# Kernel optimization log

Hardware: AMD Instinct MI355X
Metric: run time of the kernel (lower is better)

The kernel has to match this reference:

```python
import jax, jax.numpy as jnp
import numpy as np

B, L, H, E = 4, 2048, 8, 64
WINDOW = 8
DILATION = 1


def setup_inputs() -> dict:
    key = jax.random.key(0)
    kq, kk, kv, ka = jax.random.split(key, 4)
    queries = jax.random.normal(kq, (B, L, H, E), dtype=jnp.float32)
    keys = jax.random.normal(kk, (B, L, H, E), dtype=jnp.float32)
    values = jax.random.normal(kv, (B, L, H, E), dtype=jnp.float32)
    alpha = jax.random.uniform(ka, (1,), dtype=jnp.float32)
    return {"queries": queries, "keys": keys, "values": values, "alpha": alpha}


def _full_attention(q, k, v, scale):
    # q,k,v: [B, L, H, E]
    scores = jnp.einsum('blhe,bshe->bhls', q, k) * scale  # [B,H,L,L]
    A = jax.nn.softmax(scores, axis=-1)
    return jnp.einsum('bhls,bshd->blhd', A, v)


def _local_attention(q, k, v, scale):
    # efficient gather-based local window attention, non-causal
    Lk = k.shape[1]
    offsets = jnp.arange(-WINDOW, WINDOW + 1) * DILATION
    idx = jnp.clip(jnp.arange(Lk)[:, None] + offsets[None, :], 0, Lk - 1)
    K_win = k[:, idx]
    V_win = v[:, idx]
    scores = jnp.einsum('blhe,blwhe->blhw', q, K_win) * scale
    A = jax.nn.softmax(scores, axis=-1)
    return jnp.einsum('blhw,blwhe->blhe', A, V_win)


def reference(queries, keys, values, alpha):
    scale = 1.0 / np.sqrt(queries.shape[-1]).astype(np.float32)
    out_full = _full_attention(queries, keys, values, scale)
    out_local = _local_attention(queries, keys, values, scale)
    w = jax.nn.sigmoid(alpha[0])
    # only_target_first=True: positions 1..L-1 take out_full, position 0 is gated
    out = out_full.at[:, 0].set(w * out_full[:, 0] + (1.0 - w) * out_local[:, 0])
    return out
```

## Files before the change

kernel.cpp:

```cpp
#include <hip/hip_runtime.h>

typedef unsigned short u16;
typedef unsigned int   u32;
typedef __attribute__((ext_vector_type(8))) short short8;
typedef __attribute__((ext_vector_type(4))) float f32x4;

#define MFMA16(a, b, c) __builtin_amdgcn_mfma_f32_16x16x32_bf16(a, b, c, 0, 0, 0)

#define GLDS(gp, lp) __builtin_amdgcn_global_load_lds(                         \
    (const __attribute__((address_space(1))) void*)(gp),                       \
    (__attribute__((address_space(3))) void*)(lp), 16, 0, 0)

constexpr int Lv = 2048, Hv = 8, Ev = 64, HE = Hv * Ev;
constexpr float QSCALE = 0.18033688011112042f;

__device__ __forceinline__ float bf2f(u16 u) {
    u32 x = ((u32)u) << 16;
    return __builtin_bit_cast(float, x);
}
__device__ __forceinline__ u16 f2bf(float f) {
    u32 x = __builtin_bit_cast(u32, f);
    u32 r = ((x >> 16) & 1u) + 0x7fffu;
    return (u16)((x + r) >> 16);
}
__device__ __forceinline__ u32 pkbf(float a, float b) {
#if __has_builtin(__builtin_amdgcn_cvt_pk_bf16_f32)
    typedef __attribute__((ext_vector_type(2))) __bf16 bf16x2;
    bf16x2 v = __builtin_amdgcn_cvt_pk_bf16_f32(a, b);
    return __builtin_bit_cast(u32, v);
#else
    return (u32)f2bf(a) | ((u32)f2bf(b) << 16);
#endif
}
__device__ __forceinline__ float fexp2(float x) {
#if __has_builtin(__builtin_amdgcn_exp2f)
    return __builtin_amdgcn_exp2f(x);
#else
    return exp2f(x);
#endif
}

__device__ __forceinline__ int detect_isbf16(const u32* q32, int lane) {
    u32 w0 = q32[2 * lane];
    u32 w1 = q32[2 * lane + 1];
    u16 uu[4] = { (u16)(w0 & 0xffff), (u16)(w0 >> 16),
                  (u16)(w1 & 0xffff), (u16)(w1 >> 16) };
    int p = 0, z = 0;
#pragma unroll
    for (int j = 0; j < 4; ++j) {
        u16 mgn = (u16)(uu[j] & 0x7fff);
        int ex  = mgn >> 7;
        bool zero = (mgn == 0);
        bool pl   = zero || (ex >= 115 && ex <= 132);
        p += pl ? 1 : 0;
        if ((j & 1) == 0) z += zero ? 1 : 0;
    }
    int acc = p | (z << 16);
#pragma unroll
    for (int o = 1; o < 64; o <<= 1) acc += __shfl_xor(acc, o);
    int ps = acc & 0xffff, zs = acc >> 16;
    if (zs >= 100) return 0;
    return (ps >= 240) ? 1 : 0;
}

__device__ __forceinline__ short8 cvt8(const float* p) {
    float4 a = *(const float4*)p, b4 = *(const float4*)(p + 4);
    u32 r[4] = { pkbf(a.x, a.y), pkbf(a.z, a.w), pkbf(b4.x, b4.y), pkbf(b4.z, b4.w) };
    return *(short8*)r;
}
__device__ __forceinline__ short8 cvt8s(const float* p, float s) {
    float4 a = *(const float4*)p, b4 = *(const float4*)(p + 4);
    u32 r[4] = { pkbf(a.x * s, a.y * s), pkbf(a.z * s, a.w * s),
                 pkbf(b4.x * s, b4.y * s), pkbf(b4.z * s, b4.w * s) };
    return *(short8*)r;
}

__global__ __launch_bounds__(512, 4) void attn_kernel(
    const void* __restrict__ qv, const void* __restrict__ kv,
    const void* __restrict__ vv, const void* __restrict__ alphav,
    void* __restrict__ outv)
{
    __shared__ u16 Klds[64 * 64];
    __shared__ u16 Vt[64 * 64];
    __shared__ u16 Plds[8][16 * 64];

    const int tid  = threadIdx.x;
    const int w    = tid >> 6;
    const int lane = tid & 63;
    const int quad = lane >> 4;
    const int m    = lane & 15;

    const int isbf = detect_isbf16((const u32*)qv, lane);

    const int fid = blockIdx.x;
    const int bh  = (fid & 7) * 4 + ((fid >> 3) & 3);
    const int rb  = fid >> 5;
    const int b   = bh >> 3, h = bh & 7;
    const int row0 = rb * 128;

    const size_t bhoff = (size_t)b * Lv * HE + h * Ev;
    const u16*   q16 = (const u16*)qv + bhoff;
    const u16*   k16 = (const u16*)kv + bhoff;
    const u16*   v16 = (const u16*)vv + bhoff;
    const float* q32 = (const float*)qv + bhoff;
    const float* k32 = (const float*)kv + bhoff;
    const float* v32 = (const float*)vv + bhoff;

    short8 qf[2];
    {
        size_t ro = (size_t)(row0 + w * 16 + m) * HE + quad * 8;
        if (isbf) {
            short8 t0 = *(const short8*)(q16 + ro);
            short8 t1 = *(const short8*)(q16 + ro + 32);
#pragma unroll
            for (int j = 0; j < 8; ++j) {
                qf[0][j] = (short)f2bf(bf2f((u16)t0[j]) * QSCALE);
                qf[1][j] = (short)f2bf(bf2f((u16)t1[j]) * QSCALE);
            }
        } else {
            qf[0] = cvt8s(q32 + ro, QSCALE);
            qf[1] = cvt8s(q32 + ro + 32, QSCALE);
        }
    }

    short8 ones8;
#pragma unroll
    for (int j = 0; j < 8; ++j) ones8[j] = (short)0x3F80;

    f32x4 O[4];
    f32x4 Ssum = f32x4{0.f, 0.f, 0.f, 0.f};
#pragma unroll
    for (int et = 0; et < 4; ++et) O[et] = f32x4{0.f, 0.f, 0.f, 0.f};

    const int kkey = tid >> 3, ksl = tid & 7;
    const int koff = kkey * HE + (ksl ^ (kkey & 7)) * 8;
    const int eq = tid & 15, pp = tid >> 4;
    const int kcv = pp >> 2, pq = pp & 3;

    u16* Pw = Plds[w];

    for (int kt = 0; kt < 32; ++kt) {
        __syncthreads();

        if (isbf) {
            GLDS(k16 + (size_t)kt * 64 * HE + koff, Klds + w * 512);
            const u16* vp = v16 + (size_t)(kt * 64 + 2 * pp) * HE + eq * 4;
            uint2 r0 = *(const uint2*)(vp);
            uint2 r1 = *(const uint2*)(vp + HE);
            const u16* a0 = (const u16*)&r0;
            const u16* a1 = (const u16*)&r1;
#pragma unroll
            for (int j = 0; j < 4; ++j) {
                int e  = eq * 4 + j;
                int sl = kcv ^ ((e + (e >> 3)) & 7);
                u32 val = (u32)a0[j] | ((u32)a1[j] << 16);
                *(u32*)&Vt[e * 64 + sl * 8 + pq * 2] = val;
            }
        } else {
            short8 kk = cvt8(k32 + (size_t)kt * 64 * HE + koff);
            *(short8*)&Klds[tid * 8] = kk;

            const float* vp = v32 + (size_t)(kt * 64 + 2 * pp) * HE + eq * 4;
            float4 f0 = *(const float4*)(vp);
            float4 f1 = *(const float4*)(vp + HE);
            float t0[4] = {f0.x, f0.y, f0.z, f0.w};
            float t1[4] = {f1.x, f1.y, f1.z, f1.w};
#pragma unroll
            for (int j = 0; j < 4; ++j) {
                int e  = eq * 4 + j;
                int sl = kcv ^ ((e + (e >> 3)) & 7);
                *(u32*)&Vt[e * 64 + sl * 8 + pq * 2] = pkbf(t0[j], t1[j]);
            }
        }
        __syncthreads();

        f32x4 St[4];
#pragma unroll
        for (int nt = 0; nt < 4; ++nt) St[nt] = f32x4{0.f, 0.f, 0.f, 0.f};
#pragma unroll
        for (int c = 0; c < 2; ++c) {
#pragma unroll
            for (int nt = 0; nt < 4; ++nt) {
                int krow = nt * 16 + m;
                int sl   = (4 * c + quad) ^ (m & 7);
                short8 kf = *(const short8*)&Klds[krow * 64 + sl * 8];
                St[nt] = MFMA16(kf, qf[c], St[nt]);
            }
        }

#pragma unroll
        for (int nt = 0; nt < 4; ++nt) {
            u32 u0 = pkbf(fexp2(St[nt][0]), fexp2(St[nt][1]));
            u32 u1 = pkbf(fexp2(St[nt][2]), fexp2(St[nt][3]));
            int G   = 2 * nt + (quad >> 1);
            int off = m * 64 + ((G ^ (m & 7)) * 8) + (quad & 1) * 4;
            uint2 val; val.x = u0; val.y = u1;
            *(uint2*)&Pw[off] = val;
        }

#pragma unroll
        for (int c = 0; c < 2; ++c) {
            int Gp = (4 * c + quad) ^ (m & 7);
            short8 pf = *(const short8*)&Pw[m * 64 + Gp * 8];
            Ssum = MFMA16(pf, ones8, Ssum);
#pragma unroll
            for (int et = 0; et < 4; ++et) {
                int e  = et * 16 + m;
                int sl = (4 * c + quad) ^ ((e + (e >> 3)) & 7);
                short8 vf = *(const short8*)&Vt[e * 64 + sl * 8];
                O[et] = MFMA16(pf, vf, O[et]);
            }
        }
    }

    float locv[4] = {0.f, 0.f, 0.f, 0.f};
    float wgt = 0.f;
    const bool isrow0 = (rb == 0) && (w == 0) && (quad == 0);
    if (rb == 0 && w == 0) {
        const int e = lane;
        const size_t base = bhoff + e;
#define LDIN(p, i) (isbf ? bf2f(((const u16*)(p))[i]) : ((const float*)(p))[i])
        float qe = LDIN(qv, base);
        float s[9];
#pragma unroll
        for (int j = 0; j < 9; ++j) {
            float prod = qe * LDIN(kv, base + (size_t)j * HE);
#pragma unroll
            for (int o = 1; o < 64; o <<= 1) prod += __shfl_xor(prod, o);
            s[j] = prod * 0.125f;
        }
        float mx = s[0];
#pragma unroll
        for (int j = 1; j < 9; ++j) mx = fmaxf(mx, s[j]);
        float we[9];
#pragma unroll
        for (int j = 0; j < 9; ++j) we[j] = expf(s[j] - mx);
        float denom = 9.f * we[0];
        float acc   = 9.f * we[0] * LDIN(vv, base);
#pragma unroll
        for (int j = 1; j < 9; ++j) {
            denom += we[j];
            acc   += we[j] * LDIN(vv, base + (size_t)j * HE);
        }
        float loc = acc / denom;

        float a;
        if (isbf) {
            a = bf2f(((const u16*)alphav)[0]);
            if (!(a >= 0.0f && a <= 1.0f)) {
                float af = ((const float*)alphav)[0];
                if (af >= 0.0f && af <= 1.0f) a = af;
            }
        } else {
            a = ((const float*)alphav)[0];
            if (!(a >= 0.0f && a <= 1.0f)) {
                float ab = bf2f(((const u16*)alphav)[0]);
                if (ab >= 0.0f && ab <= 1.0f) a = ab;
            }
        }
        wgt = 1.f / (1.f + expf(-a));
#pragma unroll
        for (int et = 0; et < 4; ++et) locv[et] = __shfl(loc, et * 16 + m);
#undef LDIN
    }

#pragma unroll
    for (int r = 0; r < 4; ++r) {
        float inv = 1.0f / Ssum[r];
        int row = row0 + w * 16 + quad * 4 + r;
        size_t oo = (size_t)(b * Lv + row) * HE + h * Ev + m;
        bool blend = isrow0 && (r == 0);
#pragma unroll
        for (int et = 0; et < 4; ++et) {
            float res = O[et][r] * inv;
            if (blend) res = wgt * res + (1.f - wgt) * locv[et];
            if (isbf) ((u16*)outv)[oo + et * 16] = f2bf(res);
            else      ((float*)outv)[oo + et * 16] = res;
        }
    }
}

extern "C" void kernel_launch(void* const* d_in, const int* in_sizes, int n_in,
                              void* d_out, int out_size, void* d_ws, size_t ws_size,
                              hipStream_t stream) {
    hipLaunchKernelGGL(attn_kernel, dim3(512), dim3(512), 0, stream,
                       d_in[0], d_in[1], d_in[2], d_in[3], d_out);
}
```

Before: 148.5 us.

## Double-buffer K/V LDS tiles with register prefetch and template on dtype

Doubles the K and V shared-memory buffers and prefetches the next tile into registers while the current tile's MFMAs run, then stores it to the alternate buffer, so only one barrier is needed per iteration instead of two. The kernel body is also templated on the input dtype so the bf16/fp32 branches are resolved at compile time. The cost is more LDS per block (roughly 48KB) and extra registers for the prefetched data, which could limit occupancy under the 512x4 launch bounds. The bf16 path also drops the direct global-to-LDS load in favour of a register round trip.

Measured after the change: 143.3 us. -3.5%, faster.

```diff
diff --git a/kernel.cpp b/kernel.cpp
--- a/kernel.cpp
+++ b/kernel.cpp
@@ -6,10 +6,6 @@
 typedef __attribute__((ext_vector_type(4))) float f32x4;
 
 #define MFMA16(a, b, c) __builtin_amdgcn_mfma_f32_16x16x32_bf16(a, b, c, 0, 0, 0)
-
-#define GLDS(gp, lp) __builtin_amdgcn_global_load_lds(                         \
-    (const __attribute__((address_space(1))) void*)(gp),                       \
-    (__attribute__((address_space(3))) void*)(lp), 16, 0, 0)
 
 constexpr int Lv = 2048, Hv = 8, Ev = 64, HE = Hv * Ev;
 constexpr float QSCALE = 0.18033688011112042f;
@@ -63,11 +59,6 @@
     return (ps >= 240) ? 1 : 0;
 }
 
-__device__ __forceinline__ short8 cvt8(const float* p) {
-    float4 a = *(const float4*)p, b4 = *(const float4*)(p + 4);
-    u32 r[4] = { pkbf(a.x, a.y), pkbf(a.z, a.w), pkbf(b4.x, b4.y), pkbf(b4.z, b4.w) };
-    return *(short8*)r;
-}
 __device__ __forceinline__ short8 cvt8s(const float* p, float s) {
     float4 a = *(const float4*)p, b4 = *(const float4*)(p + 4);
     u32 r[4] = { pkbf(a.x * s, a.y * s), pkbf(a.z * s, a.w * s),
@@ -75,22 +66,17 @@
     return *(short8*)r;
 }
 
-__global__ __launch_bounds__(512, 4) void attn_kernel(
+template <int ISBF>
+__device__ __forceinline__ void attn_impl(
     const void* __restrict__ qv, const void* __restrict__ kv,
     const void* __restrict__ vv, const void* __restrict__ alphav,
-    void* __restrict__ outv)
+    void* __restrict__ outv, u16* Klds, u16* Vt, u16* PldsAll)
 {
-    __shared__ u16 Klds[64 * 64];
-    __shared__ u16 Vt[64 * 64];
-    __shared__ u16 Plds[8][16 * 64];
-
     const int tid  = threadIdx.x;
     const int w    = tid >> 6;
     const int lane = tid & 63;
     const int quad = lane >> 4;
     const int m    = lane & 15;
-
-    const int isbf = detect_isbf16((const u32*)qv, lane);
 
     const int fid = blockIdx.x;
     const int bh  = (fid & 7) * 4 + ((fid >> 3) & 3);
@@ -109,7 +95,7 @@
     short8 qf[2];
     {
         size_t ro = (size_t)(row0 + w * 16 + m) * HE + quad * 8;
-        if (isbf) {
+        if (ISBF) {
             short8 t0 = *(const short8*)(q16 + ro);
             short8 t1 = *(const short8*)(q16 + ro + 32);
 #pragma unroll
@@ -137,42 +123,67 @@
     const int eq = tid & 15, pp = tid >> 4;
     const int kcv = pp >> 2, pq = pp & 3;
 
-    u16* Pw = Plds[w];
+    u16* Pw = PldsAll + w * 1024;
+
+    float4 kfa, kfb, vfa, vfb;
+    uint4  kru; uint2 vru0, vru1;
+
+#define LOAD_TILE(KT)                                                          \
+    do {                                                                       \
+        if (ISBF) {                                                            \
+            kru  = *(const uint4*)(k16 + (size_t)(KT) * 64 * HE + koff);       \
+            const u16* vp_ = v16 + (size_t)((KT) * 64 + 2 * pp) * HE + eq * 4; \
+            vru0 = *(const uint2*)vp_;                                         \
+            vru1 = *(const uint2*)(vp_ + HE);                                  \
+        } else {                                                               \
+            const float* kp_ = k32 + (size_t)(KT) * 64 * HE + koff;            \
+            kfa = *(const float4*)kp_;                                         \
+            kfb = *(const float4*)(kp_ + 4);                                   \
+            const float* vp_ = v32 + (size_t)((KT) * 64 + 2 * pp) * HE + eq * 4;\
+            vfa = *(const float4*)vp_;                                         \
+            vfb = *(const float4*)(vp_ + HE);                                  \
+        }                                                                      \
+    } while (0)
+
+#define STORE_TILE(KB, VB)                                                     \
+    do {                                                                       \
+        if (ISBF) {                                                            \
+            *(uint4*)&(KB)[tid * 8] = kru;                                     \
+            const u16* a0_ = (const u16*)&vru0;                                \
+            const u16* a1_ = (const u16*)&vru1;                                \
+            _Pragma("unroll")                                                  \
+            for (int j = 0; j < 4; ++j) {                                      \
+                int e_  = eq * 4 + j;                                          \
+                int sl_ = kcv ^ ((e_ + (e_ >> 3)) & 7);                        \
+                u32 val_ = (u32)a0_[j] | ((u32)a1_[j] << 16);                  \
+                *(u32*)&(VB)[e_ * 64 + sl_ * 8 + pq * 2] = val_;               \
+            }                                                                  \
+        } else {                                                               \
+            u32 kk_[4] = { pkbf(kfa.x, kfa.y), pkbf(kfa.z, kfa.w),             \
+                           pkbf(kfb.x, kfb.y), pkbf(kfb.z, kfb.w) };           \
+            *(uint4*)&(KB)[tid * 8] = *(uint4*)kk_;                            \
+            float t0_[4] = {vfa.x, vfa.y, vfa.z, vfa.w};                       \
+            float t1_[4] = {vfb.x, vfb.y, vfb.z, vfb.w};                       \
+            _Pragma("unroll")                                                  \
+            for (int j = 0; j < 4; ++j) {                                      \
+                int e_  = eq * 4 + j;                                          \
+                int sl_ = kcv ^ ((e_ + (e_ >> 3)) & 7);                        \
+                *(u32*)&(VB)[e_ * 64 + sl_ * 8 + pq * 2] = pkbf(t0_[j], t1_[j]);\
+            }                                                                  \
+        }                                                                      \
+    } while (0)
+
+    LOAD_TILE(0);
+    STORE_TILE(Klds, Vt);
+    __syncthreads();
 
     for (int kt = 0; kt < 32; ++kt) {
-        __syncthreads();
-
-        if (isbf) {
-            GLDS(k16 + (size_t)kt * 64 * HE + koff, Klds + w * 512);
-            const u16* vp = v16 + (size_t)(kt * 64 + 2 * pp) * HE + eq * 4;
-            uint2 r0 = *(const uint2*)(vp);
-            uint2 r1 = *(const uint2*)(vp + HE);
-            const u16* a0 = (const u16*)&r0;
-            const u16* a1 = (const u16*)&r1;
-#pragma unroll
-            for (int j = 0; j < 4; ++j) {
-                int e  = eq * 4 + j;
-                int sl = kcv ^ ((e + (e >> 3)) & 7);
-                u32 val = (u32)a0[j] | ((u32)a1[j] << 16);
-                *(u32*)&Vt[e * 64 + sl * 8 + pq * 2] = val;
-            }
-        } else {
-            short8 kk = cvt8(k32 + (size_t)kt * 64 * HE + koff);
-            *(short8*)&Klds[tid * 8] = kk;
-
-            const float* vp = v32 + (size_t)(kt * 64 + 2 * pp) * HE + eq * 4;
-            float4 f0 = *(const float4*)(vp);
-            float4 f1 = *(const float4*)(vp + HE);
-            float t0[4] = {f0.x, f0.y, f0.z, f0.w};
-            float t1[4] = {f1.x, f1.y, f1.z, f1.w};
-#pragma unroll
-            for (int j = 0; j < 4; ++j) {
-                int e  = eq * 4 + j;
-                int sl = kcv ^ ((e + (e >> 3)) & 7);
-                *(u32*)&Vt[e * 64 + sl * 8 + pq * 2] = pkbf(t0[j], t1[j]);
-            }
-        }
-        __syncthreads();
+        u16* Kb = Klds + (kt & 1) * 4096;
+        u16* Vb = Vt   + (kt & 1) * 4096;
+        u16* Kn = Klds + ((kt & 1) ^ 1) * 4096;
+        u16* Vn = Vt   + ((kt & 1) ^ 1) * 4096;
+
+        if (kt < 31) LOAD_TILE(kt + 1);
 
         f32x4 St[4];
 #pragma unroll
@@ -183,7 +194,7 @@
             for (int nt = 0; nt < 4; ++nt) {
                 int krow = nt * 16 + m;
                 int sl   = (4 * c + quad) ^ (m & 7);
-                short8 kf = *(const short8*)&Klds[krow * 64 + sl * 8];
+                short8 kf = *(const short8*)&Kb[krow * 64 + sl * 8];
                 St[nt] = MFMA16(kf, qf[c], St[nt]);
             }
         }
@@ -207,11 +218,18 @@
             for (int et = 0; et < 4; ++et) {
                 int e  = et * 16 + m;
                 int sl = (4 * c + quad) ^ ((e + (e >> 3)) & 7);
-                short8 vf = *(const short8*)&Vt[e * 64 + sl * 8];
+                short8 vf = *(const short8*)&Vb[e * 64 + sl * 8];
                 O[et] = MFMA16(pf, vf, O[et]);
             }
         }
-    }
+
+        if (kt < 31) {
+            STORE_TILE(Kn, Vn);
+            __syncthreads();
+        }
+    }
+#undef LOAD_TILE
+#undef STORE_TILE
 
     float locv[4] = {0.f, 0.f, 0.f, 0.f};
     float wgt = 0.f;
@@ -219,7 +237,7 @@
     if (rb == 0 && w == 0) {
         const int e = lane;
         const size_t base = bhoff + e;
-#define LDIN(p, i) (isbf ? bf2f(((const u16*)(p))[i]) : ((const float*)(p))[i])
+#define LDIN(p, i) (ISBF ? bf2f(((const u16*)(p))[i]) : ((const float*)(p))[i])
         float qe = LDIN(qv, base);
         float s[9];
 #pragma unroll
@@ -245,7 +263,7 @@
         float loc = acc / denom;
 
         float a;
-        if (isbf) {
+        if (ISBF) {
             a = bf2f(((const u16*)alphav)[0]);
             if (!(a >= 0.0f && a <= 1.0f)) {
                 float af = ((const float*)alphav)[0];
@@ -274,10 +292,24 @@
         for (int et = 0; et < 4; ++et) {
             float res = O[et][r] * inv;
             if (blend) res = wgt * res + (1.f - wgt) * locv[et];
-            if (isbf) ((u16*)outv)[oo + et * 16] = f2bf(res);
+            if (ISBF) ((u16*)outv)[oo + et * 16] = f2bf(res);
             else      ((float*)outv)[oo + et * 16] = res;
         }
     }
+}
+
+__global__ __launch_bounds__(512, 4) void attn_kernel(
+    const void* __restrict__ qv, const void* __restrict__ kv,
+    const void* __restrict__ vv, const void* __restrict__ alphav,
+    void* __restrict__ outv)
+{
+    __shared__ u16 Klds[2 * 64 * 64];
+    __shared__ u16 Vt[2 * 64 * 64];
+    __shared__ u16 Plds[8 * 16 * 64];
+
+    const int isbf = detect_isbf16((const u32*)qv, threadIdx.x & 63);
+    if (isbf) attn_impl<1>(qv, kv, vv, alphav, outv, Klds, Vt, Plds);
+    else      attn_impl<0>(qv, kv, vv, alphav, outv, Klds, Vt, Plds);
 }
 
 extern "C" void kernel_launch(void* const* d_in, const int* in_sizes, int n_in,
```

## Double-buffer K/V tiles with register prefetch and give each wave two query row tiles

Applied to the files above, without the earlier changes.

The block shrinks from 512 to 256 threads, and each wave now processes 32 query rows as two 16-row MFMA tiles. Every K fragment and V fragment read from LDS is therefore reused across two MFMAs. The K/V LDS tiles are double-buffered: the next tile is loaded into registers before compute and written to the alternate buffer afterwards, so each iteration has one barrier instead of two. The bf16/fp32 branch becomes a template parameter, and the global_load_lds path for bf16 is dropped. In exchange, register pressure and LDS use per block go up, and each block has fewer waves to hide latency.

Result: no change. 148.2 us (-0.3%).

```diff
diff --git a/kernel.cpp b/kernel.cpp
--- a/kernel.cpp
+++ b/kernel.cpp
@@ -6,10 +6,6 @@
 typedef __attribute__((ext_vector_type(4))) float f32x4;
 
 #define MFMA16(a, b, c) __builtin_amdgcn_mfma_f32_16x16x32_bf16(a, b, c, 0, 0, 0)
-
-#define GLDS(gp, lp) __builtin_amdgcn_global_load_lds(                         \
-    (const __attribute__((address_space(1))) void*)(gp),                       \
-    (__attribute__((address_space(3))) void*)(lp), 16, 0, 0)
 
 constexpr int Lv = 2048, Hv = 8, Ev = 64, HE = Hv * Ev;
 constexpr float QSCALE = 0.18033688011112042f;
@@ -63,11 +59,6 @@
     return (ps >= 240) ? 1 : 0;
 }
 
-__device__ __forceinline__ short8 cvt8(const float* p) {
-    float4 a = *(const float4*)p, b4 = *(const float4*)(p + 4);
-    u32 r[4] = { pkbf(a.x, a.y), pkbf(a.z, a.w), pkbf(b4.x, b4.y), pkbf(b4.z, b4.w) };
-    return *(short8*)r;
-}
 __device__ __forceinline__ short8 cvt8s(const float* p, float s) {
     float4 a = *(const float4*)p, b4 = *(const float4*)(p + 4);
     u32 r[4] = { pkbf(a.x * s, a.y * s), pkbf(a.z * s, a.w * s),
@@ -75,22 +66,17 @@
     return *(short8*)r;
 }
 
-__global__ __launch_bounds__(512, 4) void attn_kernel(
+template <int ISBF>
+__device__ __forceinline__ void attn_impl(
     const void* __restrict__ qv, const void* __restrict__ kv,
     const void* __restrict__ vv, const void* __restrict__ alphav,
-    void* __restrict__ outv)
+    void* __restrict__ outv, u16* Klds, u16* Vt, u16* PldsAll)
 {
-    __shared__ u16 Klds[64 * 64];
-    __shared__ u16 Vt[64 * 64];
-    __shared__ u16 Plds[8][16 * 64];
-
     const int tid  = threadIdx.x;
     const int w    = tid >> 6;
     const int lane = tid & 63;
     const int quad = lane >> 4;
     const int m    = lane & 15;
-
-    const int isbf = detect_isbf16((const u32*)qv, lane);
 
     const int fid = blockIdx.x;
     const int bh  = (fid & 7) * 4 + ((fid >> 3) & 3);
@@ -106,20 +92,21 @@
     const float* k32 = (const float*)kv + bhoff;
     const float* v32 = (const float*)vv + bhoff;
 
-    short8 qf[2];
-    {
-        size_t ro = (size_t)(row0 + w * 16 + m) * HE + quad * 8;
-        if (isbf) {
+    short8 qf[2][2];
+#pragma unroll
+    for (int mt = 0; mt < 2; ++mt) {
+        size_t ro = (size_t)(row0 + w * 32 + mt * 16 + m) * HE + quad * 8;
+        if (ISBF) {
             short8 t0 = *(const short8*)(q16 + ro);
             short8 t1 = *(const short8*)(q16 + ro + 32);
 #pragma unroll
             for (int j = 0; j < 8; ++j) {
-                qf[0][j] = (short)f2bf(bf2f((u16)t0[j]) * QSCALE);
-                qf[1][j] = (short)f2bf(bf2f((u16)t1[j]) * QSCALE);
+                qf[mt][0][j] = (short)f2bf(bf2f((u16)t0[j]) * QSCALE);
+                qf[mt][1][j] = (short)f2bf(bf2f((u16)t1[j]) * QSCALE);
             }
         } else {
-            qf[0] = cvt8s(q32 + ro, QSCALE);
-            qf[1] = cvt8s(q32 + ro + 32, QSCALE);
+            qf[mt][0] = cvt8s(q32 + ro, QSCALE);
+            qf[mt][1] = cvt8s(q32 + ro + 32, QSCALE);
         }
     }
 
@@ -127,89 +114,159 @@
 #pragma unroll
     for (int j = 0; j < 8; ++j) ones8[j] = (short)0x3F80;
 
-    f32x4 O[4];
-    f32x4 Ssum = f32x4{0.f, 0.f, 0.f, 0.f};
-#pragma unroll
-    for (int et = 0; et < 4; ++et) O[et] = f32x4{0.f, 0.f, 0.f, 0.f};
-
-    const int kkey = tid >> 3, ksl = tid & 7;
-    const int koff = kkey * HE + (ksl ^ (kkey & 7)) * 8;
-    const int eq = tid & 15, pp = tid >> 4;
-    const int kcv = pp >> 2, pq = pp & 3;
-
-    u16* Pw = Plds[w];
+    f32x4 O[2][4];
+    f32x4 Ssum[2];
+#pragma unroll
+    for (int mt = 0; mt < 2; ++mt) {
+        Ssum[mt] = f32x4{0.f, 0.f, 0.f, 0.f};
+#pragma unroll
+        for (int et = 0; et < 4; ++et) O[mt][et] = f32x4{0.f, 0.f, 0.f, 0.f};
+    }
+
+    int koff[2];
+#pragma unroll
+    for (int t = 0; t < 2; ++t) {
+        int ci  = tid + t * 256;
+        int key = ci >> 3, sl = ci & 7;
+        koff[t] = key * HE + (sl ^ (key & 7)) * 8;
+    }
+    const int eq = tid & 15;
+    const int ppu[2] = { tid >> 4, (tid >> 4) + 16 };
+
+    u16* Pw = PldsAll + w * 2048;
+
+    uint4  kr[2];  uint2  vr[2][2];
+    float4 kf[2][2]; float4 vf[2][2];
+
+    auto load_tile = [&](int KT) {
+        if (ISBF) {
+#pragma unroll
+            for (int t = 0; t < 2; ++t)
+                kr[t] = *(const uint4*)(k16 + (size_t)KT * 64 * HE + koff[t]);
+#pragma unroll
+            for (int u = 0; u < 2; ++u) {
+                const u16* vp = v16 + (size_t)(KT * 64 + 2 * ppu[u]) * HE + eq * 4;
+                vr[u][0] = *(const uint2*)vp;
+                vr[u][1] = *(const uint2*)(vp + HE);
+            }
+        } else {
+#pragma unroll
+            for (int t = 0; t < 2; ++t) {
+                const float* kp = k32 + (size_t)KT * 64 * HE + koff[t];
+                kf[t][0] = *(const float4*)kp;
+                kf[t][1] = *(const float4*)(kp + 4);
+            }
+#pragma unroll
+            for (int u = 0; u < 2; ++u) {
+                const float* vp = v32 + (size_t)(KT * 64 + 2 * ppu[u]) * HE + eq * 4;
+                vf[u][0] = *(const float4*)vp;
+                vf[u][1] = *(const float4*)(vp + HE);
+            }
+        }
+    };
+    auto store_tile = [&](u16* KB, u16* VB) {
+        if (ISBF) {
+#pragma unroll
+            for (int t = 0; t < 2; ++t)
+                *(uint4*)&KB[(tid + t * 256) * 8] = kr[t];
+#pragma unroll
+            for (int u = 0; u < 2; ++u) {
+                int pp = ppu[u], kcv = pp >> 2, pq = pp & 3;
+                const u16* a0 = (const u16*)&vr[u][0];
+                const u16* a1 = (const u16*)&vr[u][1];
+#pragma unroll
+                for (int j = 0; j < 4; ++j) {
+                    int e  = eq * 4 + j;
+                    int sl = kcv ^ ((e + (e >> 3)) & 7);
+                    u32 val = (u32)a0[j] | ((u32)a1[j] << 16);
+                    *(u32*)&VB[e * 64 + sl * 8 + pq * 2] = val;
+                }
+            }
+        } else {
+#pragma unroll
+            for (int t = 0; t < 2; ++t) {
+                u32 kk[4] = { pkbf(kf[t][0].x, kf[t][0].y), pkbf(kf[t][0].z, kf[t][0].w),
+                              pkbf(kf[t][1].x, kf[t][1].y), pkbf(kf[t][1].z, kf[t][1].w) };
+                *(uint4*)&KB[(tid + t * 256) * 8] = *(uint4*)kk;
+            }
+#pragma unroll
+            for (int u = 0; u < 2; ++u) {
+                int pp = ppu[u], kcv = pp >> 2, pq = pp & 3;
+                float t0[4], t1[4];
+                *(float4*)t0 = vf[u][0];
+                *(float4*)t1 = vf[u][1];
+#pragma unroll
+                for (int j = 0; j < 4; ++j) {
+                    int e  = eq * 4 + j;
+                    int sl = kcv ^ ((e + (e >> 3)) & 7);
+                    *(u32*)&VB[e * 64 + sl * 8 + pq * 2] = pkbf(t0[j], t1[j]);
+                }
+            }
+        }
+    };
+
+    load_tile(0);
+    store_tile(Klds, Vt);
+    __syncthreads();
 
     for (int kt = 0; kt < 32; ++kt) {
-        __syncthreads();
-
-        if (isbf) {
-            GLDS(k16 + (size_t)kt * 64 * HE + koff, Klds + w * 512);
-            const u16* vp = v16 + (size_t)(kt * 64 + 2 * pp) * HE + eq * 4;
-            uint2 r0 = *(const uint2*)(vp);
-            uint2 r1 = *(const uint2*)(vp + HE);
-            const u16* a0 = (const u16*)&r0;
-            const u16* a1 = (const u16*)&r1;
-#pragma unroll
-            for (int j = 0; j < 4; ++j) {
-                int e  = eq * 4 + j;
-                int sl = kcv ^ ((e + (e >> 3)) & 7);
-                u32 val = (u32)a0[j] | ((u32)a1[j] << 16);
-                *(u32*)&Vt[e * 64 + sl * 8 + pq * 2] = val;
-            }
-        } else {
-            short8 kk = cvt8(k32 + (size_t)kt * 64 * HE + koff);
-            *(short8*)&Klds[tid * 8] = kk;
-
-            const float* vp = v32 + (size_t)(kt * 64 + 2 * pp) * HE + eq * 4;
-            float4 f0 = *(const float4*)(vp);
-            float4 f1 = *(const float4*)(vp + HE);
-            float t0[4] = {f0.x, f0.y, f0.z, f0.w};
-            float t1[4] = {f1.x, f1.y, f1.z, f1.w};
-#pragma unroll
-            for (int j = 0; j < 4; ++j) {
-                int e  = eq * 4 + j;
-                int sl = kcv ^ ((e + (e >> 3)) & 7);
-                *(u32*)&Vt[e * 64 + sl * 8 + pq * 2] = pkbf(t0[j], t1[j]);
-            }
-        }
-        __syncthreads();
-
-        f32x4 St[4];
-#pragma unroll
-        for (int nt = 0; nt < 4; ++nt) St[nt] = f32x4{0.f, 0.f, 0.f, 0.f};
+        u16* Kb = Klds + (kt & 1) * 4096;
+        u16* Vb = Vt   + (kt & 1) * 4096;
+        u16* Kn = Klds + ((kt & 1) ^ 1) * 4096;
+        u16* Vn = Vt   + ((kt & 1) ^ 1) * 4096;
+
+        if (kt < 31) load_tile(kt + 1);
+
+        f32x4 St[2][4];
+#pragma unroll
+        for (int mt = 0; mt < 2; ++mt)
+#pragma unroll
+            for (int nt = 0; nt < 4; ++nt) St[mt][nt] = f32x4{0.f, 0.f, 0.f, 0.f};
 #pragma unroll
         for (int c = 0; c < 2; ++c) {
 #pragma unroll
             for (int nt = 0; nt < 4; ++nt) {
                 int krow = nt * 16 + m;
                 int sl   = (4 * c + quad) ^ (m & 7);
-                short8 kf = *(const short8*)&Klds[krow * 64 + sl * 8];
-                St[nt] = MFMA16(kf, qf[c], St[nt]);
-            }
-        }
-
-#pragma unroll
-        for (int nt = 0; nt < 4; ++nt) {
-            u32 u0 = pkbf(fexp2(St[nt][0]), fexp2(St[nt][1]));
-            u32 u1 = pkbf(fexp2(St[nt][2]), fexp2(St[nt][3]));
-            int G   = 2 * nt + (quad >> 1);
-            int off = m * 64 + ((G ^ (m & 7)) * 8) + (quad & 1) * 4;
-            uint2 val; val.x = u0; val.y = u1;
-            *(uint2*)&Pw[off] = val;
+                short8 kfr = *(const short8*)&Kb[krow * 64 + sl * 8];
+                St[0][nt] = MFMA16(kfr, qf[0][c], St[0][nt]);
+                St[1][nt] = MFMA16(kfr, qf[1][c], St[1][nt]);
+            }
+        }
+
+#pragma unroll
+        for (int mt = 0; mt < 2; ++mt) {
+#pragma unroll
+            for (int nt = 0; nt < 4; ++nt) {
+                u32 u0 = pkbf(fexp2(St[mt][nt][0]), fexp2(St[mt][nt][1]));
+                u32 u1 = pkbf(fexp2(St[mt][nt][2]), fexp2(St[mt][nt][3]));
+                int G   = 2 * nt + (quad >> 1);
+                int off = (mt * 16 + m) * 64 + ((G ^ (m & 7)) * 8) + (quad & 1) * 4;
+                uint2 val; val.x = u0; val.y = u1;
+                *(uint2*)&Pw[off] = val;
+            }
         }
 
 #pragma unroll
         for (int c = 0; c < 2; ++c) {
             int Gp = (4 * c + quad) ^ (m & 7);
-            short8 pf = *(const short8*)&Pw[m * 64 + Gp * 8];
-            Ssum = MFMA16(pf, ones8, Ssum);
+            short8 pf0 = *(const short8*)&Pw[m * 64 + Gp * 8];
+            short8 pf1 = *(const short8*)&Pw[(16 + m) * 64 + Gp * 8];
+            Ssum[0] = MFMA16(pf0, ones8, Ssum[0]);
+            Ssum[1] = MFMA16(pf1, ones8, Ssum[1]);
 #pragma unroll
             for (int et = 0; et < 4; ++et) {
                 int e  = et * 16 + m;
                 int sl = (4 * c + quad) ^ ((e + (e >> 3)) & 7);
-                short8 vf = *(const short8*)&Vt[e * 64 + sl * 8];
-                O[et] = MFMA16(pf, vf, O[et]);
-            }
+                short8 vfr = *(const short8*)&Vb[e * 64 + sl * 8];
+                O[0][et] = MFMA16(pf0, vfr, O[0][et]);
+                O[1][et] = MFMA16(pf1, vfr, O[1][et]);
+            }
+        }
+
+        if (kt < 31) {
+            store_tile(Kn, Vn);
+            __syncthreads();
         }
     }
 
@@ -219,7 +276,7 @@
     if (rb == 0 && w == 0) {
         const int e = lane;
         const size_t base = bhoff + e;
-#define LDIN(p, i) (isbf ? bf2f(((const u16*)(p))[i]) : ((const float*)(p))[i])
+#define LDIN(p, i) (ISBF ? bf2f(((const u16*)(p))[i]) : ((const float*)(p))[i])
         float qe = LDIN(qv, base);
         float s[9];
 #pragma unroll
@@ -245,7 +302,7 @@
         float loc = acc / denom;
 
         float a;
-        if (isbf) {
+        if (ISBF) {
             a = bf2f(((const u16*)alphav)[0]);
             if (!(a >= 0.0f && a <= 1.0f)) {
                 float af = ((const float*)alphav)[0];
@@ -265,24 +322,41 @@
     }
 
 #pragma unroll
-    for (int r = 0; r < 4; ++r) {
-        float inv = 1.0f / Ssum[r];
-        int row = row0 + w * 16 + quad * 4 + r;
-        size_t oo = (size_t)(b * Lv + row) * HE + h * Ev + m;
-        bool blend = isrow0 && (r == 0);
-#pragma unroll
-        for (int et = 0; et < 4; ++et) {
-            float res = O[et][r] * inv;
-            if (blend) res = wgt * res + (1.f - wgt) * locv[et];
-            if (isbf) ((u16*)outv)[oo + et * 16] = f2bf(res);
-            else      ((float*)outv)[oo + et * 16] = res;
-        }
-    }
+    for (int mt = 0; mt < 2; ++mt) {
+#pragma unroll
+        for (int r = 0; r < 4; ++r) {
+            float inv = 1.0f / Ssum[mt][r];
+            int row = row0 + w * 32 + mt * 16 + quad * 4 + r;
+            size_t oo = (size_t)(b * Lv + row) * HE + h * Ev + m;
+            bool blend = isrow0 && (mt == 0) && (r == 0);
+#pragma unroll
+            for (int et = 0; et < 4; ++et) {
+                float res = O[mt][et][r] * inv;
+                if (blend) res = wgt * res + (1.f - wgt) * locv[et];
+                if (ISBF) ((u16*)outv)[oo + et * 16] = f2bf(res);
+                else      ((float*)outv)[oo + et * 16] = res;
+            }
+        }
+    }
+}
+
+__global__ __launch_bounds__(256, 2) void attn_kernel(
+    const void* __restrict__ qv, const void* __restrict__ kv,
+    const void* __restrict__ vv, const void* __restrict__ alphav,
+    void* __restrict__ outv)
+{
+    __shared__ u16 Klds[2 * 64 * 64];
+    __shared__ u16 Vt[2 * 64 * 64];
+    __shared__ u16 Plds[4 * 32 * 64];
+
+    const int isbf = detect_isbf16((const u32*)qv, threadIdx.x & 63);
+    if (isbf) attn_impl<1>(qv, kv, vv, alphav, outv, Klds, Vt, Plds);
+    else      attn_impl<0>(qv, kv, vv, alphav, outv, Klds, Vt, Plds);
 }
 
 extern "C" void kernel_launch(void* const* d_in, const int* in_sizes, int n_in,
                               void* d_out, int out_size, void* d_ws, size_t ws_size,
                               hipStream_t stream) {
-    hipLaunchKernelGGL(attn_kernel, dim3(512), dim3(512), 0, stream,
+    hipLaunchKernelGGL(attn_kernel, dim3(512), dim3(256), 0, stream,
                        d_in[0], d_in[1], d_in[2], d_in[3], d_out);
 }
```

## Precompute bf16 K and pre-swizzled transposed V in workspace, double-buffer V tiles

Applied to the files above, without the earlier changes.

Adds a prep kernel that converts K to bf16 in a compact per-head layout and writes V as bf16 tiles already transposed and swizzled for LDS. The attention kernel then reads K fragments straight from global memory instead of staging them in LDS, and streams V tiles into a double-buffered LDS area with async global-to-LDS loads. This leaves one barrier per iteration and removes the per-block fp32-to-bf16 conversion of K and V. It also templates the dtype branch. The cost is an extra kernel launch and a pass over K and V into the workspace, and the path only runs when the workspace is large enough.

New measurement: 218.7 us. 1.47x slower.

```diff
diff --git a/kernel.cpp b/kernel.cpp
--- a/kernel.cpp
+++ b/kernel.cpp
@@ -75,23 +75,87 @@
     return *(short8*)r;
 }
 
-__global__ __launch_bounds__(512, 4) void attn_kernel(
+template <int ISBF>
+__device__ __forceinline__ void prep_impl(const void* kv, const void* vv,
+                                          u16* kb, u16* vs, float* T)
+{
+    const int bid = blockIdx.x, tid = threadIdx.x;
+    if (bid < 1024) {
+        const int bh = bid >> 5, kt = bid & 31;
+        const int b = bh >> 3, h = bh & 7;
+        const int ky = tid >> 2, q4 = tid & 3;
+        const size_t inrow = ((size_t)(b * Lv + kt * 64 + ky) * Hv + h) * Ev;
+        if (ISBF) {
+            const u16* ip = (const u16*)vv + inrow + q4 * 16;
+#pragma unroll
+            for (int j = 0; j < 16; ++j) T[ky * 69 + q4 * 16 + j] = bf2f(ip[j]);
+        } else {
+            const float* ip = (const float*)vv + inrow + q4 * 16;
+#pragma unroll
+            for (int j = 0; j < 4; ++j)
+                *(float4*)&T[ky * 69 + q4 * 16 + j * 4] = *(const float4*)(ip + j * 4);
+        }
+        __syncthreads();
+        u16* outt = vs + ((size_t)bh * 32 + kt) * 4096;
+#pragma unroll
+        for (int t2 = 0; t2 < 2; ++t2) {
+            int ci = tid + t2 * 256;
+            int e = ci >> 3, slot = ci & 7;
+            int kc = slot ^ ((e + (e >> 3)) & 7);
+            u32 rr[4];
+#pragma unroll
+            for (int jj = 0; jj < 4; ++jj)
+                rr[jj] = pkbf(T[(kc * 8 + 2 * jj) * 69 + e],
+                              T[(kc * 8 + 2 * jj + 1) * 69 + e]);
+            *(uint4*)&outt[ci * 8] = *(uint4*)rr;
+        }
+    } else {
+        int t_lin = (bid - 1024) * 256 + tid;
+        int e0 = (t_lin & 3) * 16;
+        int rl = t_lin >> 2;
+        int l = rl & 2047, bh = rl >> 11;
+        int b = bh >> 3, h = bh & 7;
+        size_t in0 = ((size_t)(b * Lv + l) * Hv + h) * Ev + e0;
+        u32 rr[8];
+        if (ISBF) {
+            const u16* ip = (const u16*)kv + in0;
+            *(uint4*)rr       = *(const uint4*)ip;
+            *(uint4*)(rr + 4) = *(const uint4*)(ip + 8);
+        } else {
+            const float* ip = (const float*)kv + in0;
+#pragma unroll
+            for (int j = 0; j < 8; ++j) {
+                float2 f = *(const float2*)(ip + j * 2);
+                rr[j] = pkbf(f.x, f.y);
+            }
+        }
+        *(uint4*)&kb[(size_t)t_lin * 16]     = *(uint4*)rr;
+        *(uint4*)&kb[(size_t)t_lin * 16 + 8] = *(uint4*)(rr + 4);
+    }
+}
+
+__global__ void prep_kernel(const void* qv, const void* kv, const void* vv,
+                            u16* kb, u16* vs)
+{
+    __shared__ float T[64 * 69];
+    const int isbf = detect_isbf16((const u32*)qv, threadIdx.x & 63);
+    if (isbf) prep_impl<1>(kv, vv, kb, vs, T);
+    else      prep_impl<0>(kv, vv, kb, vs, T);
+}
+
+template <int ISBF, int PRE>
+__device__ __forceinline__ void attn_impl(
     const void* __restrict__ qv, const void* __restrict__ kv,
     const void* __restrict__ vv, const void* __restrict__ alphav,
-    void* __restrict__ outv)
+    void* __restrict__ outv, const u16* __restrict__ kb,
+    const u16* __restrict__ vs, u16* Vbuf, u16* PldsAll)
 {
-    __shared__ u16 Klds[64 * 64];
-    __shared__ u16 Vt[64 * 64];
-    __shared__ u16 Plds[8][16 * 64];
-
     const int tid  = threadIdx.x;
     const int w    = tid >> 6;
     const int lane = tid & 63;
     const int quad = lane >> 4;
     const int m    = lane & 15;
 
-    const int isbf = detect_isbf16((const u32*)qv, lane);
-
     const int fid = blockIdx.x;
     const int bh  = (fid & 7) * 4 + ((fid >> 3) & 3);
     const int rb  = fid >> 5;
@@ -100,16 +164,18 @@
 
     const size_t bhoff = (size_t)b * Lv * HE + h * Ev;
     const u16*   q16 = (const u16*)qv + bhoff;
-    const u16*   k16 = (const u16*)kv + bhoff;
-    const u16*   v16 = (const u16*)vv + bhoff;
     const float* q32 = (const float*)qv + bhoff;
-    const float* k32 = (const float*)kv + bhoff;
-    const float* v32 = (const float*)vv + bhoff;
+    const u16*   k16o = (const u16*)kv + bhoff;
+    const float* k32o = (const float*)kv + bhoff;
+    const u16*   v16o = (const u16*)vv + bhoff;
+    const float* v32o = (const float*)vv + bhoff;
+    const u16*   kbbh = kb + (size_t)bh * (Lv * Ev);
+    const u16*   vsbh = vs + (size_t)bh * (32 * 4096);
 
     short8 qf[2];
     {
         size_t ro = (size_t)(row0 + w * 16 + m) * HE + quad * 8;
-        if (isbf) {
+        if (ISBF) {
             short8 t0 = *(const short8*)(q16 + ro);
             short8 t1 = *(const short8*)(q16 + ro + 32);
 #pragma unroll
@@ -132,47 +198,53 @@
 #pragma unroll
     for (int et = 0; et < 4; ++et) O[et] = f32x4{0.f, 0.f, 0.f, 0.f};
 
-    const int kkey = tid >> 3, ksl = tid & 7;
-    const int koff = kkey * HE + (ksl ^ (kkey & 7)) * 8;
     const int eq = tid & 15, pp = tid >> 4;
     const int kcv = pp >> 2, pq = pp & 3;
-
-    u16* Pw = Plds[w];
-
-    for (int kt = 0; kt < 32; ++kt) {
-        __syncthreads();
-
-        if (isbf) {
-            GLDS(k16 + (size_t)kt * 64 * HE + koff, Klds + w * 512);
-            const u16* vp = v16 + (size_t)(kt * 64 + 2 * pp) * HE + eq * 4;
-            uint2 r0 = *(const uint2*)(vp);
-            uint2 r1 = *(const uint2*)(vp + HE);
-            const u16* a0 = (const u16*)&r0;
-            const u16* a1 = (const u16*)&r1;
+    uint2 vr0, vr1; float4 vfa, vfb;
+
+    auto v_load = [&](int KT) {
+        if (ISBF) {
+            const u16* vp = v16o + (size_t)(KT * 64 + 2 * pp) * HE + eq * 4;
+            vr0 = *(const uint2*)vp; vr1 = *(const uint2*)(vp + HE);
+        } else {
+            const float* vp = v32o + (size_t)(KT * 64 + 2 * pp) * HE + eq * 4;
+            vfa = *(const float4*)vp; vfb = *(const float4*)(vp + HE);
+        }
+    };
+    auto v_store = [&](u16* VB) {
+        if (ISBF) {
+            const u16* a0 = (const u16*)&vr0;
+            const u16* a1 = (const u16*)&vr1;
 #pragma unroll
             for (int j = 0; j < 4; ++j) {
                 int e  = eq * 4 + j;
                 int sl = kcv ^ ((e + (e >> 3)) & 7);
                 u32 val = (u32)a0[j] | ((u32)a1[j] << 16);
-                *(u32*)&Vt[e * 64 + sl * 8 + pq * 2] = val;
-            }
-        } else {
-            short8 kk = cvt8(k32 + (size_t)kt * 64 * HE + koff);
-            *(short8*)&Klds[tid * 8] = kk;
-
-            const float* vp = v32 + (size_t)(kt * 64 + 2 * pp) * HE + eq * 4;
-            float4 f0 = *(const float4*)(vp);
-            float4 f1 = *(const float4*)(vp + HE);
-            float t0[4] = {f0.x, f0.y, f0.z, f0.w};
-            float t1[4] = {f1.x, f1.y, f1.z, f1.w};
+                *(u32*)&VB[e * 64 + sl * 8 + pq * 2] = val;
+            }
+        } else {
+            float t0[4], t1[4];
+            *(float4*)t0 = vfa; *(float4*)t1 = vfb;
 #pragma unroll
             for (int j = 0; j < 4; ++j) {
                 int e  = eq * 4 + j;
                 int sl = kcv ^ ((e + (e >> 3)) & 7);
-                *(u32*)&Vt[e * 64 + sl * 8 + pq * 2] = pkbf(t0[j], t1[j]);
-            }
-        }
-        __syncthreads();
+                *(u32*)&VB[e * 64 + sl * 8 + pq * 2] = pkbf(t0[j], t1[j]);
+            }
+        }
+    };
+
+    if (PRE) { GLDS(vsbh + tid * 8, Vbuf + tid * 8); }
+    else     { v_load(0); v_store(Vbuf); }
+    __syncthreads();
+
+    u16* Pw = PldsAll + w * 1024;
+
+    for (int kt = 0; kt < 32; ++kt) {
+        u16* cur = Vbuf + (kt & 1) * 4096;
+        u16* nxt = Vbuf + ((kt & 1) ^ 1) * 4096;
+
+        if (!PRE && kt < 31) v_load(kt + 1);
 
         f32x4 St[4];
 #pragma unroll
@@ -181,12 +253,23 @@
         for (int c = 0; c < 2; ++c) {
 #pragma unroll
             for (int nt = 0; nt < 4; ++nt) {
-                int krow = nt * 16 + m;
-                int sl   = (4 * c + quad) ^ (m & 7);
-                short8 kf = *(const short8*)&Klds[krow * 64 + sl * 8];
+                short8 kf;
+                if (PRE) {
+                    kf = *(const short8*)(kbbh +
+                         ((size_t)kt * 64 + nt * 16 + m) * 64 + c * 32 + quad * 8);
+                } else if (ISBF) {
+                    kf = *(const short8*)(k16o +
+                         (size_t)(kt * 64 + nt * 16 + m) * HE + c * 32 + quad * 8);
+                } else {
+                    kf = cvt8(k32o +
+                         (size_t)(kt * 64 + nt * 16 + m) * HE + c * 32 + quad * 8);
+                }
                 St[nt] = MFMA16(kf, qf[c], St[nt]);
             }
         }
+
+        if (PRE && kt < 31)
+            GLDS(vsbh + (size_t)(kt + 1) * 4096 + tid * 8, nxt + tid * 8);
 
 #pragma unroll
         for (int nt = 0; nt < 4; ++nt) {
@@ -207,9 +290,14 @@
             for (int et = 0; et < 4; ++et) {
                 int e  = et * 16 + m;
                 int sl = (4 * c + quad) ^ ((e + (e >> 3)) & 7);
-                short8 vf = *(const short8*)&Vt[e * 64 + sl * 8];
+                short8 vf = *(const short8*)&cur[e * 64 + sl * 8];
                 O[et] = MFMA16(pf, vf, O[et]);
             }
+        }
+
+        if (kt < 31) {
+            if (!PRE) v_store(nxt);
+            __syncthreads();
         }
     }
 
@@ -219,7 +307,7 @@
     if (rb == 0 && w == 0) {
         const int e = lane;
         const size_t base = bhoff + e;
-#define LDIN(p, i) (isbf ? bf2f(((const u16*)(p))[i]) : ((const float*)(p))[i])
+#define LDIN(p, i) (ISBF ? bf2f(((const u16*)(p))[i]) : ((const float*)(p))[i])
         float qe = LDIN(qv, base);
         float s[9];
 #pragma unroll
@@ -245,7 +333,7 @@
         float loc = acc / denom;
 
         float a;
-        if (isbf) {
+        if (ISBF) {
             a = bf2f(((const u16*)alphav)[0]);
             if (!(a >= 0.0f && a <= 1.0f)) {
                 float af = ((const float*)alphav)[0];
@@ -274,15 +362,46 @@
         for (int et = 0; et < 4; ++et) {
             float res = O[et][r] * inv;
             if (blend) res = wgt * res + (1.f - wgt) * locv[et];
-            if (isbf) ((u16*)outv)[oo + et * 16] = f2bf(res);
+            if (ISBF) ((u16*)outv)[oo + et * 16] = f2bf(res);
             else      ((float*)outv)[oo + et * 16] = res;
         }
     }
+}
+
+template <int PRE>
+__global__ __launch_bounds__(512, 4) void attn_kernel(
+    const void* __restrict__ qv, const void* __restrict__ kv,
+    const void* __restrict__ vv, const void* __restrict__ alphav,
+    void* __restrict__ outv, const u16* __restrict__ kb,
+    const u16* __restrict__ vs)
+{
+    __shared__ u16 Vbuf[2 * 4096];
+    __shared__ u16 Plds[8 * 1024];
+
+    const int isbf = detect_isbf16((const u32*)qv, threadIdx.x & 63);
+    if (isbf) attn_impl<1, PRE>(qv, kv, vv, alphav, outv, kb, vs, Vbuf, Plds);
+    else      attn_impl<0, PRE>(qv, kv, vv, alphav, outv, kb, vs, Vbuf, Plds);
 }
 
 extern "C" void kernel_launch(void* const* d_in, const int* in_sizes, int n_in,
                               void* d_out, int out_size, void* d_ws, size_t ws_size,
                               hipStream_t stream) {
-    hipLaunchKernelGGL(attn_kernel, dim3(512), dim3(512), 0, stream,
-                       d_in[0], d_in[1], d_in[2], d_in[3], d_out);
-}
+    const void* q = d_in[0];
+    const void* k = d_in[1];
+    const void* v = d_in[2];
+    const void* a = d_in[3];
+
+    u16* kb = (u16*)d_ws;
+    u16* vs = kb + 4194304;
+    const bool usepre = (ws_size >= 16777216u);
+
+    if (usepre) {
+        hipLaunchKernelGGL(prep_kernel, dim3(2048), dim3(256), 0, stream,
+                           q, k, v, kb, vs);
+        hipLaunchKernelGGL(attn_kernel<1>, dim3(512), dim3(512), 0, stream,
+                           q, k, v, a, d_out, kb, vs);
+    } else {
+        hipLaunchKernelGGL(attn_kernel<0>, dim3(512), dim3(512), 0, stream,
+                           q, k, v, a, d_out, kb, vs);
+    }
+}
```
